# Performance work log

Measured on AMD Instinct MI355X. Metric: run time of the kernel, lower is better.

Reference implementation:

```python
import jax, jax.numpy as jnp
import numpy as np
from jax import lax

EPS = 1e-5
DW_THRESH = 4.0
PW_THRESH = 1e-3


def setup_inputs() -> dict:
    key = jax.random.key(0)
    ks = jax.random.split(key, 13)
    B, C, O, H, W = 32, 256, 256, 56, 56
    inp = {
        "x": jax.random.normal(ks[0], (B, C, H, W), jnp.float32),
        "dw_w": jax.random.normal(ks[1], (C, 1, 3, 3), jnp.float32) * 0.2,
        "dw_b": jax.random.normal(ks[2], (C,), jnp.float32) * 0.1,
        "bn1_gamma": 0.5 + jax.random.uniform(ks[3], (C,), jnp.float32) * 1.5,
        "bn1_beta": jax.random.normal(ks[4], (C,), jnp.float32) * 0.5,
        "bn1_mean": jax.random.normal(ks[5], (C,), jnp.float32) * 0.1,
        "bn1_var": 0.5 + jax.random.uniform(ks[6], (C,), jnp.float32),
        "pw_w": jax.random.normal(ks[7], (O, C, 1, 1), jnp.float32) * 0.06,
        "pw_b": jax.random.normal(ks[8], (O,), jnp.float32) * 0.1,
        "bn2_gamma": 0.5 + jax.random.uniform(ks[9], (O,), jnp.float32) * 1.5,
        "bn2_beta": jax.random.normal(ks[10], (O,), jnp.float32) * 0.5,
        "bn2_mean": jax.random.normal(ks[11], (O,), jnp.float32) * 0.1,
        "bn2_var": 0.5 + jax.random.uniform(ks[12], (O,), jnp.float32),
    }
    return inp


def _bn(x, gamma, beta, mean, var):
    # inference-mode BatchNorm2d over channel axis 1
    inv = gamma * lax.rsqrt(var + EPS)
    return x * inv[None, :, None, None] + (beta - mean * inv)[None, :, None, None]


def _cut(x, thresh):
    # per-(batch, channel) max-abs pruning: max(max(x), -min(x)) == max(|x|)
    max_abs = jnp.max(jnp.abs(x), axis=(2, 3))  # [B, C]
    return jnp.where((max_abs < thresh)[:, :, None, None], 0.0, x)


def reference(x, dw_w, dw_b, bn1_gamma, bn1_beta, bn1_mean, bn1_var,
              pw_w, pw_b, bn2_gamma, bn2_beta, bn2_mean, bn2_var):
    C = x.shape[1]
    # depthwise 3x3 conv, padding=1, groups=C
    y = lax.conv_general_dilated(
        x, dw_w, window_strides=(1, 1), padding=[(1, 1), (1, 1)],
        feature_group_count=C,
        dimension_numbers=("NCHW", "OIHW", "NCHW"),
    ) + dw_b[None, :, None, None]
    y = jax.nn.relu(_bn(y, bn1_gamma, bn1_beta, bn1_mean, bn1_var))
    y = _cut(y, DW_THRESH)
    # pointwise 1x1 conv as channel contraction
    z = jnp.einsum("bihw,oi->bohw", y, pw_w[:, :, 0, 0]) + pw_b[None, :, None, None]
    z = jax.nn.relu(_bn(z, bn2_gamma, bn2_beta, bn2_mean, bn2_var))
    z = _cut(z, PW_THRESH)
    return z
```

## Files before the change

kernel.cpp:

```cpp
#include <hip/hip_runtime.h>
#include <hip/hip_bf16.h>
#include <stdint.h>

#define BATCH 32
#define CIN   256
#define COUT  256
#define HW    3136
#define NPAD  3200

typedef short bf16x8 __attribute__((ext_vector_type(8)));
typedef float f32x4  __attribute__((ext_vector_type(4)));

__device__ __forceinline__ unsigned short f2bf(float f) {
    unsigned u = __float_as_uint(f);
    u += 0x7fffu + ((u >> 16) & 1u);
    return (unsigned short)(u >> 16);
}

__global__ __launch_bounds__(256) void prep_kernel(
        const float* __restrict__ pw_w, const float* __restrict__ pw_b,
        const float* __restrict__ g2, const float* __restrict__ be2,
        const float* __restrict__ mu2, const float* __restrict__ va2,
        unsigned short* __restrict__ Wp, float* __restrict__ b2,
        unsigned* __restrict__ pwmax, unsigned* __restrict__ dwmax) {
    int o = blockIdx.x;
    int t = threadIdx.x;
    float inv2 = g2[o] * rsqrtf(va2[o] + 1e-5f);
    Wp[o * CIN + t] = f2bf(pw_w[o * CIN + t] * inv2);
    if (t == 0) b2[o] = pw_b[o] * inv2 + be2[o] - mu2[o] * inv2;
    int idx = blockIdx.x * 256 + t;
    if (idx < BATCH * COUT) { pwmax[idx] = 0u; dwmax[idx] = 0u; }
}

__global__ __launch_bounds__(256) void dw_kernel(
        const float* __restrict__ x, const float* __restrict__ dww,
        const float* __restrict__ dwb,
        const float* __restrict__ g1, const float* __restrict__ be1,
        const float* __restrict__ mu1, const float* __restrict__ va1,
        unsigned short* __restrict__ y, unsigned* __restrict__ dwmax) {
    int blk = blockIdx.x;
    int c = blk & 255;
    int b = blk >> 8;
    int tid = threadIdx.x;
    const float* xp = x + (size_t)(b * CIN + c) * HW;

    float w00 = dww[c*9+0], w01 = dww[c*9+1], w02 = dww[c*9+2];
    float w10 = dww[c*9+3], w11 = dww[c*9+4], w12 = dww[c*9+5];
    float w20 = dww[c*9+6], w21 = dww[c*9+7], w22 = dww[c*9+8];
    float inv = g1[c] * rsqrtf(va1[c] + 1e-5f);
    float b0  = dwb[c] * inv + (be1[c] - mu1[c] * inv);

    float vals[4][4];
    float lmax = 0.f;
#pragma unroll
    for (int i = 0; i < 4; ++i) {
        int q = tid + i * 256;
        bool qv = (i < 3) || (tid < 16);
        int qq = qv ? q : 783;
        int h = qq / 14;
        int c0 = (qq - h * 14) * 4;
        float a0 = 0.f, a1 = 0.f, a2 = 0.f, a3 = 0.f;
#pragma unroll
        for (int r = 0; r < 3; ++r) {
            int gr = h + r - 1;
            bool rv = (unsigned)gr < 56u;
            int grc = gr < 0 ? 0 : (gr > 55 ? 55 : gr);
            const float* rowp = xp + grc * 56;
            float4 vv = *(const float4*)(rowp + c0);
            float s0 = (rv && c0 != 0) ? rowp[c0 - 1] : 0.f;
            float s5 = (rv && c0 < 52) ? rowp[c0 + 4] : 0.f;
            float s1 = rv ? vv.x : 0.f;
            float s2 = rv ? vv.y : 0.f;
            float s3 = rv ? vv.z : 0.f;
            float s4 = rv ? vv.w : 0.f;
            float wl = r == 0 ? w00 : (r == 1 ? w10 : w20);
            float wc = r == 0 ? w01 : (r == 1 ? w11 : w21);
            float wr = r == 0 ? w02 : (r == 1 ? w12 : w22);
            a0 = fmaf(s0, wl, fmaf(s1, wc, fmaf(s2, wr, a0)));
            a1 = fmaf(s1, wl, fmaf(s2, wc, fmaf(s3, wr, a1)));
            a2 = fmaf(s2, wl, fmaf(s3, wc, fmaf(s4, wr, a2)));
            a3 = fmaf(s3, wl, fmaf(s4, wc, fmaf(s5, wr, a3)));
        }
        float v0 = fmaxf(fmaf(a0, inv, b0), 0.f);
        float v1 = fmaxf(fmaf(a1, inv, b0), 0.f);
        float v2 = fmaxf(fmaf(a2, inv, b0), 0.f);
        float v3 = fmaxf(fmaf(a3, inv, b0), 0.f);
        vals[i][0] = v0; vals[i][1] = v1; vals[i][2] = v2; vals[i][3] = v3;
        if (qv)
            lmax = fmaxf(lmax, fmaxf(fmaxf(v0, v1), fmaxf(v2, v3)));
    }

    for (int off = 32; off >= 1; off >>= 1)
        lmax = fmaxf(lmax, __shfl_xor(lmax, off, 64));
    if ((tid & 63) == 0) atomicMax(&dwmax[blk], __float_as_uint(lmax));

    unsigned short* yp = y + (size_t)(b * CIN + c) * NPAD;
#pragma unroll
    for (int i = 0; i < 4; ++i) {
        int q = tid + i * 256;
        if ((i < 3) || (tid < 16)) {
            ushort4 o;
            o.x = f2bf(vals[i][0]); o.y = f2bf(vals[i][1]);
            o.z = f2bf(vals[i][2]); o.w = f2bf(vals[i][3]);
            *(ushort4*)(yp + q * 4) = o;
        }
    }
    if (tid < 16) *(ushort4*)(yp + HW + tid * 4) = make_ushort4(0, 0, 0, 0);
}

__global__ __launch_bounds__(256) void pw_kernel(
        const unsigned short* __restrict__ y, const unsigned short* __restrict__ Wp,
        const float* __restrict__ b2, const float* __restrict__ dwm,
        float* __restrict__ z, unsigned* __restrict__ pwmax) {
    __shared__ __align__(16) unsigned short Al[128 * 64];
    __shared__ __align__(16) unsigned short Bl[128 * 64];

    int bid = blockIdx.x;
    int mt = bid & 1;
    int rest = bid >> 1;
    int nt = rest % 25;
    int b = rest / 25;
    int m0 = mt * 128, n0 = nt * 128;

    int tid = threadIdx.x;
    int lane = tid & 63, wid = tid >> 6;
    int wm = (wid & 1) * 64, wn = (wid >> 1) * 64;
    int l15 = lane & 15, l4 = lane >> 4;

    const unsigned short* yb = y + (size_t)b * CIN * NPAD;
    const float* dwb_ = dwm + b * 256;

    int am[4], acch[4];
    const unsigned short* asrc[4];
#pragma unroll
    for (int i = 0; i < 4; ++i) {
        int s = i * 256 + tid;
        int m = s >> 3, cch = s & 7, dch = cch ^ (m & 7);
        am[i] = m; acch[i] = cch;
        asrc[i] = Wp + (size_t)(m0 + m) * CIN + dch * 8;
    }
    int bq[2], bnq[2];
    const unsigned short* bsrc[2];
#pragma unroll
    for (int i = 0; i < 2; ++i) {
        int u = tid + i * 256;
        bq[i] = u >> 5; bnq[i] = u & 31;
        bsrc[i] = yb + (size_t)(bq[i] * 4) * NPAD + n0 + bnq[i] * 4;
    }

    uint4 areg[4];
    uint2 breg[2][4];
    float4 fl[2];
#pragma unroll
    for (int i = 0; i < 4; ++i) areg[i] = *(const uint4*)(asrc[i]);
#pragma unroll
    for (int i = 0; i < 2; ++i) {
#pragma unroll
        for (int r = 0; r < 4; ++r) breg[i][r] = *(const uint2*)(bsrc[i] + r * NPAD);
        fl[i] = *(const float4*)(dwb_ + bq[i] * 4);
    }

    f32x4 acc[4][4];
#pragma unroll
    for (int mf = 0; mf < 4; ++mf)
#pragma unroll
        for (int nf = 0; nf < 4; ++nf) acc[mf][nf] = {0.f, 0.f, 0.f, 0.f};

#pragma unroll
    for (int kk = 0; kk < 4; ++kk) {
        __builtin_amdgcn_s_barrier();
        __builtin_amdgcn_sched_barrier(0);
#pragma unroll
        for (int i = 0; i < 4; ++i)
            *(uint4*)((char*)Al + am[i] * 128 + acch[i] * 16) = areg[i];
#pragma unroll
        for (int i = 0; i < 2; ++i) {
            unsigned mk0 = fl[i].x >= 4.0f ? 0xffffffffu : 0u;
            unsigned mk1 = fl[i].y >= 4.0f ? 0xffffffffu : 0u;
            unsigned mk2 = fl[i].z >= 4.0f ? 0xffffffffu : 0u;
            unsigned mk3 = fl[i].w >= 4.0f ? 0xffffffffu : 0u;
            uint2 r0 = breg[i][0], r1 = breg[i][1], r2 = breg[i][2], r3 = breg[i][3];
            r0.x &= mk0; r0.y &= mk0; r1.x &= mk1; r1.y &= mk1;
            r2.x &= mk2; r2.y &= mk2; r3.x &= mk3; r3.y &= mk3;
            int q = bq[i], nq = bnq[i];
#pragma unroll
            for (int i2 = 0; i2 < 4; ++i2) {
                unsigned x0 = (i2 & 2) ? r0.y : r0.x;
                unsigned x1 = (i2 & 2) ? r1.y : r1.x;
                unsigned x2 = (i2 & 2) ? r2.y : r2.x;
                unsigned x3 = (i2 & 2) ? r3.y : r3.x;
                if (i2 & 1) { x0 >>= 16; x2 >>= 16; }
                else        { x0 &= 0xffffu; x2 &= 0xffffu; }
                unsigned px = (i2 & 1) ? (x0 | (x1 & 0xffff0000u))
                                       : (x0 | (x1 << 16));
                unsigned py = (i2 & 1) ? (x2 | (x3 & 0xffff0000u))
                                       : (x2 | (x3 << 16));
                int nloc = nq * 4 + i2;
                int sb = nloc * 128 + (((q >> 1) ^ ((nloc >> 2) & 7)) << 4) + ((q & 1) << 3);
                *(uint2*)((char*)Bl + sb) = make_uint2(px, py);
            }
        }
        if (kk < 3) {
#pragma unroll
            for (int i = 0; i < 4; ++i)
                areg[i] = *(const uint4*)(asrc[i] + (kk + 1) * 64);
#pragma unroll
            for (int i = 0; i < 2; ++i) {
#pragma unroll
                for (int r = 0; r < 4; ++r)
                    breg[i][r] = *(const uint2*)(bsrc[i] + (size_t)(kk + 1) * 64 * NPAD + r * NPAD);
                fl[i] = *(const float4*)(dwb_ + (kk + 1) * 64 + bq[i] * 4);
            }
        }
        asm volatile("s_waitcnt lgkmcnt(0)" ::: "memory");
        __builtin_amdgcn_s_barrier();
        __builtin_amdgcn_sched_barrier(0);
#pragma unroll
        for (int h = 0; h < 2; ++h) {
            bf16x8 af[4], bfr[4];
            int cc = h * 4 + l4;
#pragma unroll
            for (int mf = 0; mf < 4; ++mf) {
                int m = wm + mf * 16 + l15;
                af[mf] = *(const bf16x8*)((const char*)Al + m * 128 + ((cc ^ (m & 7)) << 4));
            }
#pragma unroll
            for (int nf = 0; nf < 4; ++nf) {
                int n = wn + nf * 16 + l15;
                bfr[nf] = *(const bf16x8*)((const char*)Bl + n * 128 + ((cc ^ ((n >> 2) & 7)) << 4));
            }
#pragma unroll
            for (int mf = 0; mf < 4; ++mf)
#pragma unroll
                for (int nf = 0; nf < 4; ++nf)
                    acc[mf][nf] = __builtin_amdgcn_mfma_f32_16x16x32_bf16(
                        af[mf], bfr[nf], acc[mf][nf], 0, 0, 0);
        }
    }

    float* zb = z + (size_t)b * COUT * HW;
#pragma unroll
    for (int mf = 0; mf < 4; ++mf) {
        int obase = m0 + wm + mf * 16 + l4 * 4;
        float bb0 = b2[obase + 0], bb1 = b2[obase + 1];
        float bb2v = b2[obase + 2], bb3 = b2[obase + 3];
        float rmax[4] = {0.f, 0.f, 0.f, 0.f};
#pragma unroll
        for (int nf = 0; nf < 4; ++nf) {
            int n = n0 + wn + nf * 16 + l15;
            bool valid = (n < HW);
            float v0 = fmaxf(acc[mf][nf][0] + bb0, 0.f);
            float v1 = fmaxf(acc[mf][nf][1] + bb1, 0.f);
            float v2 = fmaxf(acc[mf][nf][2] + bb2v, 0.f);
            float v3 = fmaxf(acc[mf][nf][3] + bb3, 0.f);
            if (valid) {
                zb[(size_t)(obase + 0) * HW + n] = v0;
                zb[(size_t)(obase + 1) * HW + n] = v1;
                zb[(size_t)(obase + 2) * HW + n] = v2;
                zb[(size_t)(obase + 3) * HW + n] = v3;
                rmax[0] = fmaxf(rmax[0], v0);
                rmax[1] = fmaxf(rmax[1], v1);
                rmax[2] = fmaxf(rmax[2], v2);
                rmax[3] = fmaxf(rmax[3], v3);
            }
        }
#pragma unroll
        for (int r = 0; r < 4; ++r) {
            float v = rmax[r];
            v = fmaxf(v, __shfl_xor(v, 1, 64));
            v = fmaxf(v, __shfl_xor(v, 2, 64));
            v = fmaxf(v, __shfl_xor(v, 4, 64));
            v = fmaxf(v, __shfl_xor(v, 8, 64));
            if (l15 == 0)
                atomicMax(&pwmax[b * COUT + obase + r], __float_as_uint(v));
        }
    }
}

__global__ __launch_bounds__(256) void cut_kernel(const unsigned* __restrict__ pwmax,
                                                  float* __restrict__ z) {
    int base = blockIdx.x * 8;
#pragma unroll
    for (int j = 0; j < 8; ++j) {
        int bo = base + j;
        if (__uint_as_float(pwmax[bo]) >= 1e-3f) continue;
        float4* zp = (float4*)(z + (size_t)bo * HW);
        for (int i = threadIdx.x; i < HW / 4; i += 256)
            zp[i] = make_float4(0.f, 0.f, 0.f, 0.f);
    }
}

extern "C" void kernel_launch(void* const* d_in, const int* in_sizes, int n_in,
                              void* d_out, int out_size, void* d_ws, size_t ws_size,
                              hipStream_t stream) {
    const float* x   = (const float*)d_in[0];
    const float* dww = (const float*)d_in[1];
    const float* dwb = (const float*)d_in[2];
    const float* g1  = (const float*)d_in[3];
    const float* be1 = (const float*)d_in[4];
    const float* mu1 = (const float*)d_in[5];
    const float* va1 = (const float*)d_in[6];
    const float* pww = (const float*)d_in[7];
    const float* pwb = (const float*)d_in[8];
    const float* g2  = (const float*)d_in[9];
    const float* be2 = (const float*)d_in[10];
    const float* mu2 = (const float*)d_in[11];
    const float* va2 = (const float*)d_in[12];
    float* z = (float*)d_out;

    char* ws = (char*)d_ws;
    const size_t Y_BYTES = (size_t)BATCH * CIN * NPAD * 2;
    unsigned short* y  = (unsigned short*)ws;
    unsigned short* Wp = (unsigned short*)(ws + Y_BYTES);
    float* b2          = (float*)(ws + Y_BYTES + 131072);
    unsigned* pwmax    = (unsigned*)(ws + Y_BYTES + 131072 + 1024);
    unsigned* dwmax    = (unsigned*)(ws + Y_BYTES + 131072 + 1024 + 32768);

    prep_kernel<<<256, 256, 0, stream>>>(pww, pwb, g2, be2, mu2, va2, Wp, b2, pwmax, dwmax);
    dw_kernel<<<BATCH * CIN, 256, 0, stream>>>(x, dww, dwb, g1, be1, mu1, va1, y, dwmax);
    pw_kernel<<<2 * 25 * BATCH, 256, 0, stream>>>(y, Wp, b2, (const float*)dwmax, z, pwmax);
    cut_kernel<<<BATCH * COUT / 8, 256, 0, stream>>>(pwmax, z);
}
```

Measured before the change: 120.4 us.

## Rewrite depthwise kernel with row-sliding register reuse and multi-plane blocks

The depthwise conv kernel now handles 8 planes per block. Each thread covers an 8-column by 14-row band and slides a 3-row register window, so every input row is loaded once instead of three times. The per-plane max is reduced through shared memory and written directly, which removes the atomics and the zero-initialisation in prep. The pointwise GEMM block index is also remapped to spread tiles across XCDs. The risks are 32 idle threads per block, higher register pressure (launch bounds set to 3 blocks), and fewer blocks in flight.

```diff
diff --git a/kernel.cpp b/kernel.cpp
--- a/kernel.cpp
+++ b/kernel.cpp
@@ -22,90 +22,120 @@
         const float* __restrict__ g2, const float* __restrict__ be2,
         const float* __restrict__ mu2, const float* __restrict__ va2,
         unsigned short* __restrict__ Wp, float* __restrict__ b2,
-        unsigned* __restrict__ pwmax, unsigned* __restrict__ dwmax) {
+        unsigned* __restrict__ pwmax) {
     int o = blockIdx.x;
     int t = threadIdx.x;
     float inv2 = g2[o] * rsqrtf(va2[o] + 1e-5f);
     Wp[o * CIN + t] = f2bf(pw_w[o * CIN + t] * inv2);
     if (t == 0) b2[o] = pw_b[o] * inv2 + be2[o] - mu2[o] * inv2;
     int idx = blockIdx.x * 256 + t;
-    if (idx < BATCH * COUT) { pwmax[idx] = 0u; dwmax[idx] = 0u; }
-}
-
-__global__ __launch_bounds__(256) void dw_kernel(
+    if (idx < BATCH * COUT) pwmax[idx] = 0u;
+}
+
+#define LOADROW(dst, rp, mrow) do {                                        \
+    float4 v0_ = *(const float4*)((rp) + c0);                              \
+    float4 v1_ = *(const float4*)((rp) + c0 + 4);                          \
+    dst[0] = (rp)[lidx] * (msL * (mrow));                                  \
+    dst[1] = v0_.x * (mrow); dst[2] = v0_.y * (mrow);                      \
+    dst[3] = v0_.z * (mrow); dst[4] = v0_.w * (mrow);                      \
+    dst[5] = v1_.x * (mrow); dst[6] = v1_.y * (mrow);                      \
+    dst[7] = v1_.z * (mrow); dst[8] = v1_.w * (mrow);                      \
+    dst[9] = (rp)[ridx] * (msR * (mrow));                                  \
+} while (0)
+
+__global__ __launch_bounds__(256, 3) void dw_kernel(
         const float* __restrict__ x, const float* __restrict__ dww,
         const float* __restrict__ dwb,
         const float* __restrict__ g1, const float* __restrict__ be1,
         const float* __restrict__ mu1, const float* __restrict__ va1,
-        unsigned short* __restrict__ y, unsigned* __restrict__ dwmax) {
+        unsigned short* __restrict__ y, float* __restrict__ dwmax) {
+    int tid = threadIdx.x;
     int blk = blockIdx.x;
-    int c = blk & 255;
-    int b = blk >> 8;
-    int tid = threadIdx.x;
-    const float* xp = x + (size_t)(b * CIN + c) * HW;
-
-    float w00 = dww[c*9+0], w01 = dww[c*9+1], w02 = dww[c*9+2];
-    float w10 = dww[c*9+3], w11 = dww[c*9+4], w12 = dww[c*9+5];
-    float w20 = dww[c*9+6], w21 = dww[c*9+7], w22 = dww[c*9+8];
-    float inv = g1[c] * rsqrtf(va1[c] + 1e-5f);
-    float b0  = dwb[c] * inv + (be1[c] - mu1[c] * inv);
-
-    float vals[4][4];
+    __shared__ float lmx[256];
+
     float lmax = 0.f;
-#pragma unroll
-    for (int i = 0; i < 4; ++i) {
-        int q = tid + i * 256;
-        bool qv = (i < 3) || (tid < 16);
-        int qq = qv ? q : 783;
-        int h = qq / 14;
-        int c0 = (qq - h * 14) * 4;
-        float a0 = 0.f, a1 = 0.f, a2 = 0.f, a3 = 0.f;
-#pragma unroll
-        for (int r = 0; r < 3; ++r) {
-            int gr = h + r - 1;
-            bool rv = (unsigned)gr < 56u;
-            int grc = gr < 0 ? 0 : (gr > 55 ? 55 : gr);
-            const float* rowp = xp + grc * 56;
-            float4 vv = *(const float4*)(rowp + c0);
-            float s0 = (rv && c0 != 0) ? rowp[c0 - 1] : 0.f;
-            float s5 = (rv && c0 < 52) ? rowp[c0 + 4] : 0.f;
-            float s1 = rv ? vv.x : 0.f;
-            float s2 = rv ? vv.y : 0.f;
-            float s3 = rv ? vv.z : 0.f;
-            float s4 = rv ? vv.w : 0.f;
-            float wl = r == 0 ? w00 : (r == 1 ? w10 : w20);
-            float wc = r == 0 ? w01 : (r == 1 ? w11 : w21);
-            float wr = r == 0 ? w02 : (r == 1 ? w12 : w22);
-            a0 = fmaf(s0, wl, fmaf(s1, wc, fmaf(s2, wr, a0)));
-            a1 = fmaf(s1, wl, fmaf(s2, wc, fmaf(s3, wr, a1)));
-            a2 = fmaf(s2, wl, fmaf(s3, wc, fmaf(s4, wr, a2)));
-            a3 = fmaf(s3, wl, fmaf(s4, wc, fmaf(s5, wr, a3)));
-        }
-        float v0 = fmaxf(fmaf(a0, inv, b0), 0.f);
-        float v1 = fmaxf(fmaf(a1, inv, b0), 0.f);
-        float v2 = fmaxf(fmaf(a2, inv, b0), 0.f);
-        float v3 = fmaxf(fmaf(a3, inv, b0), 0.f);
-        vals[i][0] = v0; vals[i][1] = v1; vals[i][2] = v2; vals[i][3] = v3;
-        if (qv)
-            lmax = fmaxf(lmax, fmaxf(fmaxf(v0, v1), fmaxf(v2, v3)));
-    }
-
-    for (int off = 32; off >= 1; off >>= 1)
-        lmax = fmaxf(lmax, __shfl_xor(lmax, off, 64));
-    if ((tid & 63) == 0) atomicMax(&dwmax[blk], __float_as_uint(lmax));
-
-    unsigned short* yp = y + (size_t)(b * CIN + c) * NPAD;
-#pragma unroll
-    for (int i = 0; i < 4; ++i) {
-        int q = tid + i * 256;
-        if ((i < 3) || (tid < 16)) {
-            ushort4 o;
-            o.x = f2bf(vals[i][0]); o.y = f2bf(vals[i][1]);
-            o.z = f2bf(vals[i][2]); o.w = f2bf(vals[i][3]);
-            *(ushort4*)(yp + q * 4) = o;
-        }
-    }
-    if (tid < 16) *(ushort4*)(yp + HW + tid * 4) = make_ushort4(0, 0, 0, 0);
+    if (tid < 224) {
+        int p    = tid / 28;
+        int r28  = tid - p * 28;
+        int band = r28 / 7;
+        int sc   = r28 - band * 7;
+        int plane = blk * 8 + p;
+        int c = plane & 255;
+        int r0 = band * 14;
+        int c0 = sc * 8;
+
+        const float* xq = x + (size_t)plane * HW;
+        float w00 = dww[c*9+0], w01 = dww[c*9+1], w02 = dww[c*9+2];
+        float w10 = dww[c*9+3], w11 = dww[c*9+4], w12 = dww[c*9+5];
+        float w20 = dww[c*9+6], w21 = dww[c*9+7], w22 = dww[c*9+8];
+        float inv = g1[c] * rsqrtf(va1[c] + 1e-5f);
+        float b0  = dwb[c] * inv + (be1[c] - mu1[c] * inv);
+
+        float msL  = (sc == 0) ? 0.f : 1.f;
+        float msR  = (sc == 6) ? 0.f : 1.f;
+        int   lidx = (sc == 0) ? c0 : c0 - 1;
+        int   ridx = (sc == 6) ? c0 + 7 : c0 + 8;
+        float mTop = (band == 0) ? 0.f : 1.f;
+        float mBot = (band == 3) ? 0.f : 1.f;
+
+        float A[10], Bv[10], Cv[10], nx[10];
+        {
+            const float* rp = xq + ((band == 0) ? 0 : (r0 - 1)) * 56;
+            LOADROW(A, rp, mTop);
+        }
+        {
+            const float* rp = xq + r0 * 56;
+            LOADROW(Bv, rp, 1.f);
+        }
+        {
+            const float* rp = xq + (r0 + 1) * 56;
+            LOADROW(nx, rp, 1.f);
+        }
+        unsigned short* yq = y + (size_t)plane * NPAD + c0;
+
+#pragma unroll
+        for (int i = 0; i < 14; ++i) {
+#pragma unroll
+            for (int t2 = 0; t2 < 10; ++t2) Cv[t2] = nx[t2];
+            if (i < 13) {
+                const float* rp = xq + ((i == 12) ? ((band == 3) ? 55 : (r0 + 14))
+                                                  : (r0 + i + 2)) * 56;
+                if (i == 12) { LOADROW(nx, rp, mBot); }
+                else         { LOADROW(nx, rp, 1.f); }
+            }
+            unsigned us[8];
+#pragma unroll
+            for (int j = 0; j < 8; ++j) {
+                float o = fmaf(A[j],    w00, fmaf(A[j+1],  w01, fmaf(A[j+2],  w02,
+                          fmaf(Bv[j],   w10, fmaf(Bv[j+1], w11, fmaf(Bv[j+2], w12,
+                          fmaf(Cv[j],   w20, fmaf(Cv[j+1], w21, Cv[j+2] * w22))))))));
+                float v = fmaxf(fmaf(o, inv, b0), 0.f);
+                lmax = fmaxf(lmax, v);
+                us[j] = f2bf(v);
+            }
+            uint4 st;
+            st.x = us[0] | (us[1] << 16);
+            st.y = us[2] | (us[3] << 16);
+            st.z = us[4] | (us[5] << 16);
+            st.w = us[6] | (us[7] << 16);
+            *(uint4*)(yq + (r0 + i) * 56) = st;
+#pragma unroll
+            for (int t2 = 0; t2 < 10; ++t2) { A[t2] = Bv[t2]; Bv[t2] = Cv[t2]; }
+        }
+    }
+    lmx[tid] = lmax;
+    __syncthreads();
+    if (tid < 8) {
+        float m = 0.f;
+#pragma unroll 4
+        for (int j = 0; j < 28; ++j) m = fmaxf(m, lmx[tid * 28 + j]);
+        dwmax[blk * 8 + tid] = m;
+    }
+    if (tid < 64) {
+        int p = tid >> 3;
+        uint4* dst = (uint4*)(y + (size_t)(blk * 8 + p) * NPAD + HW) + (tid & 7);
+        *dst = make_uint4(0, 0, 0, 0);
+    }
 }
 
 __global__ __launch_bounds__(256) void pw_kernel(
@@ -115,7 +145,8 @@
     __shared__ __align__(16) unsigned short Al[128 * 64];
     __shared__ __align__(16) unsigned short Bl[128 * 64];
 
-    int bid = blockIdx.x;
+    int bid0 = blockIdx.x;
+    int bid = (bid0 & 7) * 200 + (bid0 >> 3);
     int mt = bid & 1;
     int rest = bid >> 1;
     int nt = rest % 25;
@@ -314,10 +345,10 @@
     unsigned short* Wp = (unsigned short*)(ws + Y_BYTES);
     float* b2          = (float*)(ws + Y_BYTES + 131072);
     unsigned* pwmax    = (unsigned*)(ws + Y_BYTES + 131072 + 1024);
-    unsigned* dwmax    = (unsigned*)(ws + Y_BYTES + 131072 + 1024 + 32768);
-
-    prep_kernel<<<256, 256, 0, stream>>>(pww, pwb, g2, be2, mu2, va2, Wp, b2, pwmax, dwmax);
-    dw_kernel<<<BATCH * CIN, 256, 0, stream>>>(x, dww, dwb, g1, be1, mu1, va1, y, dwmax);
-    pw_kernel<<<2 * 25 * BATCH, 256, 0, stream>>>(y, Wp, b2, (const float*)dwmax, z, pwmax);
+    float* dwmax       = (float*)(ws + Y_BYTES + 131072 + 1024 + 32768);
+
+    prep_kernel<<<256, 256, 0, stream>>>(pww, pwb, g2, be2, mu2, va2, Wp, b2, pwmax);
+    dw_kernel<<<1024, 256, 0, stream>>>(x, dww, dwb, g1, be1, mu1, va1, y, dwmax);
+    pw_kernel<<<1600, 256, 0, stream>>>(y, Wp, b2, dwmax, z, pwmax);
     cut_kernel<<<BATCH * COUT / 8, 256, 0, stream>>>(pwmax, z);
 }
```

New measurement: 112.6 us. -6.4%, faster.

## Rewrite depthwise conv as one wave per plane with rolling row accumulators

Applied to the files above, without the earlier changes.

The depthwise kernel now assigns one 64-lane wave to each (batch, channel) plane. Each lane owns a column and walks down the rows, getting horizontal neighbours through lane shuffles and keeping two rolling partial sums, so every input element is loaded once instead of roughly three times. Because a plane is handled by a single wave, the per-plane max is written directly and the atomicMax and the zero-initialisation in prep are no longer needed. The pointwise GEMM block index is also remapped so consecutive blocks land on different XCDs. In exchange, the bf16 stores become scalar 2-byte writes and 8 of the 64 lanes in each wave sit idle.

```diff
diff --git a/kernel.cpp b/kernel.cpp
--- a/kernel.cpp
+++ b/kernel.cpp
@@ -22,14 +22,14 @@
         const float* __restrict__ g2, const float* __restrict__ be2,
         const float* __restrict__ mu2, const float* __restrict__ va2,
         unsigned short* __restrict__ Wp, float* __restrict__ b2,
-        unsigned* __restrict__ pwmax, unsigned* __restrict__ dwmax) {
+        unsigned* __restrict__ pwmax) {
     int o = blockIdx.x;
     int t = threadIdx.x;
     float inv2 = g2[o] * rsqrtf(va2[o] + 1e-5f);
     Wp[o * CIN + t] = f2bf(pw_w[o * CIN + t] * inv2);
     if (t == 0) b2[o] = pw_b[o] * inv2 + be2[o] - mu2[o] * inv2;
     int idx = blockIdx.x * 256 + t;
-    if (idx < BATCH * COUT) { pwmax[idx] = 0u; dwmax[idx] = 0u; }
+    if (idx < BATCH * COUT) pwmax[idx] = 0u;
 }
 
 __global__ __launch_bounds__(256) void dw_kernel(
@@ -37,12 +37,16 @@
         const float* __restrict__ dwb,
         const float* __restrict__ g1, const float* __restrict__ be1,
         const float* __restrict__ mu1, const float* __restrict__ va1,
-        unsigned short* __restrict__ y, unsigned* __restrict__ dwmax) {
-    int blk = blockIdx.x;
-    int c = blk & 255;
-    int b = blk >> 8;
-    int tid = threadIdx.x;
-    const float* xp = x + (size_t)(b * CIN + c) * HW;
+        unsigned short* __restrict__ y, float* __restrict__ dwmax) {
+    int lane = threadIdx.x & 63;
+    int wid  = threadIdx.x >> 6;
+    int plane = blockIdx.x * 4 + wid;
+    int c = plane & 255;
+
+    int col = lane < 56 ? lane : 55;
+    bool active = lane < 56;
+    const float* xp = x + (size_t)plane * HW + col;
+    unsigned short* yp = y + (size_t)plane * NPAD + col;
 
     float w00 = dww[c*9+0], w01 = dww[c*9+1], w02 = dww[c*9+2];
     float w10 = dww[c*9+3], w11 = dww[c*9+4], w12 = dww[c*9+5];
@@ -50,62 +54,40 @@
     float inv = g1[c] * rsqrtf(va1[c] + 1e-5f);
     float b0  = dwb[c] * inv + (be1[c] - mu1[c] * inv);
 
-    float vals[4][4];
+    float A = 0.f;
+    float B = 0.f;
     float lmax = 0.f;
-#pragma unroll
-    for (int i = 0; i < 4; ++i) {
-        int q = tid + i * 256;
-        bool qv = (i < 3) || (tid < 16);
-        int qq = qv ? q : 783;
-        int h = qq / 14;
-        int c0 = (qq - h * 14) * 4;
-        float a0 = 0.f, a1 = 0.f, a2 = 0.f, a3 = 0.f;
-#pragma unroll
-        for (int r = 0; r < 3; ++r) {
-            int gr = h + r - 1;
-            bool rv = (unsigned)gr < 56u;
-            int grc = gr < 0 ? 0 : (gr > 55 ? 55 : gr);
-            const float* rowp = xp + grc * 56;
-            float4 vv = *(const float4*)(rowp + c0);
-            float s0 = (rv && c0 != 0) ? rowp[c0 - 1] : 0.f;
-            float s5 = (rv && c0 < 52) ? rowp[c0 + 4] : 0.f;
-            float s1 = rv ? vv.x : 0.f;
-            float s2 = rv ? vv.y : 0.f;
-            float s3 = rv ? vv.z : 0.f;
-            float s4 = rv ? vv.w : 0.f;
-            float wl = r == 0 ? w00 : (r == 1 ? w10 : w20);
-            float wc = r == 0 ? w01 : (r == 1 ? w11 : w21);
-            float wr = r == 0 ? w02 : (r == 1 ? w12 : w22);
-            a0 = fmaf(s0, wl, fmaf(s1, wc, fmaf(s2, wr, a0)));
-            a1 = fmaf(s1, wl, fmaf(s2, wc, fmaf(s3, wr, a1)));
-            a2 = fmaf(s2, wl, fmaf(s3, wc, fmaf(s4, wr, a2)));
-            a3 = fmaf(s3, wl, fmaf(s4, wc, fmaf(s5, wr, a3)));
-        }
-        float v0 = fmaxf(fmaf(a0, inv, b0), 0.f);
-        float v1 = fmaxf(fmaf(a1, inv, b0), 0.f);
-        float v2 = fmaxf(fmaf(a2, inv, b0), 0.f);
-        float v3 = fmaxf(fmaf(a3, inv, b0), 0.f);
-        vals[i][0] = v0; vals[i][1] = v1; vals[i][2] = v2; vals[i][3] = v3;
-        if (qv)
-            lmax = fmaxf(lmax, fmaxf(fmaxf(v0, v1), fmaxf(v2, v3)));
-    }
-
+
+#pragma unroll
+    for (int q = 0; q < 56; ++q) {
+        float xv = xp[q * 56];
+        float xl = __shfl_up(xv, 1, 64);
+        float xr = __shfl_down(xv, 1, 64);
+        if (lane == 0)  xl = 0.f;
+        if (lane >= 55) xr = 0.f;
+        float outv = fmaf(xl, w20, fmaf(xv, w21, fmaf(xr, w22, A)));
+        A = fmaf(xl, w10, fmaf(xv, w11, fmaf(xr, w12, B)));
+        B = fmaf(xl, w00, fmaf(xv, w01, xr * w02));
+        if (q >= 1) {
+            float v = fmaxf(fmaf(outv, inv, b0), 0.f);
+            if (active) {
+                lmax = fmaxf(lmax, v);
+                yp[(q - 1) * 56] = f2bf(v);
+            }
+        }
+    }
+    {
+        float v = fmaxf(fmaf(A, inv, b0), 0.f);
+        if (active) {
+            lmax = fmaxf(lmax, v);
+            yp[55 * 56] = f2bf(v);
+        }
+    }
     for (int off = 32; off >= 1; off >>= 1)
         lmax = fmaxf(lmax, __shfl_xor(lmax, off, 64));
-    if ((tid & 63) == 0) atomicMax(&dwmax[blk], __float_as_uint(lmax));
-
-    unsigned short* yp = y + (size_t)(b * CIN + c) * NPAD;
-#pragma unroll
-    for (int i = 0; i < 4; ++i) {
-        int q = tid + i * 256;
-        if ((i < 3) || (tid < 16)) {
-            ushort4 o;
-            o.x = f2bf(vals[i][0]); o.y = f2bf(vals[i][1]);
-            o.z = f2bf(vals[i][2]); o.w = f2bf(vals[i][3]);
-            *(ushort4*)(yp + q * 4) = o;
-        }
-    }
-    if (tid < 16) *(ushort4*)(yp + HW + tid * 4) = make_ushort4(0, 0, 0, 0);
+    if (lane == 0) dwmax[plane] = lmax;
+    if (lane < 8) *(uint4*)(y + (size_t)plane * NPAD + HW + lane * 8)
+        = make_uint4(0, 0, 0, 0);
 }
 
 __global__ __launch_bounds__(256) void pw_kernel(
@@ -115,7 +97,8 @@
     __shared__ __align__(16) unsigned short Al[128 * 64];
     __shared__ __align__(16) unsigned short Bl[128 * 64];
 
-    int bid = blockIdx.x;
+    int bid0 = blockIdx.x;
+    int bid = (bid0 & 7) * 200 + (bid0 >> 3);
     int mt = bid & 1;
     int rest = bid >> 1;
     int nt = rest % 25;
@@ -314,10 +297,10 @@
     unsigned short* Wp = (unsigned short*)(ws + Y_BYTES);
     float* b2          = (float*)(ws + Y_BYTES + 131072);
     unsigned* pwmax    = (unsigned*)(ws + Y_BYTES + 131072 + 1024);
-    unsigned* dwmax    = (unsigned*)(ws + Y_BYTES + 131072 + 1024 + 32768);
-
-    prep_kernel<<<256, 256, 0, stream>>>(pww, pwb, g2, be2, mu2, va2, Wp, b2, pwmax, dwmax);
-    dw_kernel<<<BATCH * CIN, 256, 0, stream>>>(x, dww, dwb, g1, be1, mu1, va1, y, dwmax);
-    pw_kernel<<<2 * 25 * BATCH, 256, 0, stream>>>(y, Wp, b2, (const float*)dwmax, z, pwmax);
+    float* dwmax       = (float*)(ws + Y_BYTES + 131072 + 1024 + 32768);
+
+    prep_kernel<<<256, 256, 0, stream>>>(pww, pwb, g2, be2, mu2, va2, Wp, b2, pwmax);
+    dw_kernel<<<2048, 256, 0, stream>>>(x, dww, dwb, g1, be1, mu1, va1, y, dwmax);
+    pw_kernel<<<1600, 256, 0, stream>>>(y, Wp, b2, dwmax, z, pwmax);
     cut_kernel<<<BATCH * COUT / 8, 256, 0, stream>>>(pwmax, z);
 }
```

New measurement: 110.6 us. 8.1% less time.
